# Optimization experiments

Measured on AMD Instinct MI355X. Metric: run time of the kernel, lower is better.

Reference implementation:

```python
import jax, jax.numpy as jnp
import numpy as np

KERNEL_SIZE = 5  # k, local correlation window
EPS = 1e-6


def local_self_correlation(x, k):
    """x: (b,c,h,w) -> (b,k^2,h,w). For each of the k^2 shifts (dy,dx) compute
    sum_c x[..., y+dy, x+dx] * x[..., y, x] with zero padding at borders."""
    pad = k // 2
    b, c, h, w = x.shape
    xp = jnp.pad(x, ((0, 0), (0, 0), (pad, pad), (pad, pad)))
    outs = []
    for dy in range(-pad, pad + 1):  # fixed small loop over k^2 shifts
        for dx in range(-pad, pad + 1):
            nb = xp[:, :, pad + dy:pad + dy + h, pad + dx:pad + dx + w]
            outs.append(jnp.sum(nb * x, axis=1))  # (b,h,w)
    return jnp.stack(outs, axis=1)  # (b,k^2,h,w)


def feature_l2norm(f):
    norm = jnp.sqrt(jnp.sum(f * f, axis=1, keepdims=True) + EPS)
    return f / norm


def setup_inputs() -> dict:
    key = jax.random.key(0)
    k1, k2, k3 = jax.random.split(key, 3)
    b, c, h, w = 8, 1024, 64, 64
    hidden = 1024
    in_dim = c + KERNEL_SIZE * KERNEL_SIZE  # 1049
    x = jax.random.normal(k1, (b, c, h, w), dtype=jnp.float32)
    W = jax.random.normal(k2, (hidden, in_dim), dtype=jnp.float32) * 0.02
    bias = jax.random.normal(k3, (hidden,), dtype=jnp.float32) * 0.02
    return {"x": x, "W": W, "b": bias}


def reference(x, W, b):
    feature_gs = local_self_correlation(x, KERNEL_SIZE)      # (b,k^2,h,w)
    feature_gs = feature_l2norm(feature_gs)
    feature_cat = jnp.concatenate([x, feature_gs], axis=1)    # (b,c+k^2,h,w)
    # 1x1 conv == channel GEMM, then ReLU
    out = jnp.einsum('bihw,oi->bohw', feature_cat, W) + b[None, :, None, None]
    return jax.nn.relu(out)
```

## Files before the change

kernel.cpp:

```cpp
#include <hip/hip_runtime.h>

typedef __attribute__((ext_vector_type(8))) short bf16x8;
typedef __attribute__((ext_vector_type(4))) float f32x4;

__device__ __forceinline__ unsigned short f2bf(float f) {
    unsigned int u = __float_as_uint(f);
    unsigned int r = (u + 0x7fffu + ((u >> 16) & 1u)) >> 16;
    return (unsigned short)r;
}

#define KPAD 1088
#define NT   17

__global__ void kWb_conv(const float* __restrict__ W, unsigned short* __restrict__ Wb)
{
    const int o = blockIdx.x;
    for (int k = threadIdx.x; k < KPAD; k += 256) {
        float v = (k < 1049) ? W[(size_t)o * 1049 + k] : 0.f;
        Wb[(size_t)o * KPAD + k] = f2bf(v);
    }
}

__global__ __launch_bounds__(256) void kT_conv(const float* __restrict__ x,
                                               unsigned short* __restrict__ xT)
{
    __shared__ unsigned short tile[64][128];
    const int bid = blockIdx.x;
    const int mst = bid >> 3;
    const int ct  = bid & 7;
    const int m0  = mst * 64;
    const int b   = m0 >> 12, ms0 = m0 & 4095;
    const int t   = threadIdx.x;
    const int msq = (t & 15) * 4;
    const int cg  = t >> 4;
    const int c0  = ct * 128 + cg * 8;

    const float* src = x + ((size_t)b * 1024 + c0) * 4096 + ms0 + msq;
    float4 v[8];
    #pragma unroll
    for (int j = 0; j < 8; ++j)
        v[j] = *(const float4*)(src + (size_t)j * 4096);

    #pragma unroll
    for (int p = 0; p < 4; ++p) {
        unsigned int w[4];
        #pragma unroll
        for (int q = 0; q < 4; ++q) {
            float lo = ((const float*)&v[2 * q])[p];
            float hi = ((const float*)&v[2 * q + 1])[p];
            w[q] = (unsigned int)f2bf(lo) | ((unsigned int)f2bf(hi) << 16);
        }
        const int row = msq + p;
        const int pch = cg ^ ((row >> 2) & 15);
        *(uint4*)&tile[row][pch * 8] = make_uint4(w[0], w[1], w[2], w[3]);
    }
    __syncthreads();

    #pragma unroll
    for (int q = 0; q < 4; ++q) {
        const int flat = q * 256 + t;
        const int row  = flat >> 4, ch = flat & 15;
        const int pch  = ch ^ ((row >> 2) & 15);
        uint4 val = *(const uint4*)&tile[row][pch * 8];
        *(uint4*)((char*)xT + (size_t)(m0 + row) * (KPAD * 2) + (size_t)(ct * 128 + ch * 8) * 2) = val;
    }
}

__global__ __launch_bounds__(256, 2) void k1a_corr(const float* __restrict__ x,
                                                   float* __restrict__ fpart)
{
    __shared__ float slab[2][20][68];
    const int bid   = blockIdx.x;
    const int split = bid & 15;
    const int b     = (bid >> 4) & 7;
    const int rg    = bid >> 7;
    const int y0    = rg * 16;
    const int t     = threadIdx.x;
    const int tc    = t & 15, tr = t >> 4;
    const int cs    = tc * 4;

    if (t < 160) {
        int buf = t / 80, rem = t % 80;
        int r = rem >> 2, cc = rem & 3;
        slab[buf][r][(cc < 2) ? cc : (64 + cc)] = 0.f;
    }

    float acc[25][4];
    #pragma unroll
    for (int s = 0; s < 25; ++s)
        #pragma unroll
        for (int p = 0; p < 4; ++p) acc[s][p] = 0.f;

    const float* xb = x + ((size_t)b * 1024 + split * 64) * 4096;

    const int r0 = t >> 4,         c40 = t & 15;
    const int y0r0 = y0 - 2 + r0;
    const int r1 = (t + 256) >> 4, c41 = t & 15;
    const int y0r1 = y0 - 2 + r1;
    const bool has1 = (t < 64);

    #define K1A_LOAD(ch, VA, VB)                                                \
        {                                                                        \
            const float* s_ = xb + (size_t)(ch) * 4096;                          \
            VA = (y0r0 >= 0 && y0r0 < 64) ? *(const float4*)(s_ + y0r0 * 64 + c40 * 4) \
                                          : make_float4(0.f, 0.f, 0.f, 0.f);     \
            if (has1)                                                            \
                VB = (y0r1 >= 0 && y0r1 < 64) ? *(const float4*)(s_ + y0r1 * 64 + c41 * 4) \
                                              : make_float4(0.f, 0.f, 0.f, 0.f); \
        }
    #define K1A_WRITE(buf, VA, VB)                                               \
        {                                                                        \
            float2* d0 = (float2*)&slab[buf][r0][2 + c40 * 4];                   \
            d0[0] = make_float2(VA.x, VA.y);                                     \
            d0[1] = make_float2(VA.z, VA.w);                                     \
            if (has1) {                                                          \
                float2* d1 = (float2*)&slab[buf][r1][2 + c41 * 4];               \
                d1[0] = make_float2(VB.x, VB.y);                                 \
                d1[1] = make_float2(VB.z, VB.w);                                 \
            }                                                                    \
        }
    #define K1A_COMPUTE(buf)                                                     \
        {                                                                        \
            const float* base = &slab[buf][tr][cs];                              \
            float ctr[4], wf[8];                                                 \
            {                                                                    \
                const float4* pr = (const float4*)(base + 2 * 68);               \
                float4 a = pr[0], b4 = pr[1];                                    \
                wf[0]=a.x; wf[1]=a.y; wf[2]=a.z; wf[3]=a.w;                      \
                wf[4]=b4.x; wf[5]=b4.y; wf[6]=b4.z; wf[7]=b4.w;                  \
                ctr[0]=wf[2]; ctr[1]=wf[3]; ctr[2]=wf[4]; ctr[3]=wf[5];          \
                _Pragma("unroll")                                                \
                for (int dx = -2; dx <= 2; ++dx)                                 \
                    _Pragma("unroll")                                            \
                    for (int p = 0; p < 4; ++p)                                  \
                        acc[10 + dx + 2][p] += wf[p + 2 + dx] * ctr[p];          \
            }                                                                    \
            _Pragma("unroll")                                                    \
            for (int r = 0; r < 5; ++r) {                                        \
                if (r == 2) continue;                                            \
                const float4* pr = (const float4*)(base + r * 68);               \
                float4 a = pr[0], b4 = pr[1];                                    \
                wf[0]=a.x; wf[1]=a.y; wf[2]=a.z; wf[3]=a.w;                      \
                wf[4]=b4.x; wf[5]=b4.y; wf[6]=b4.z; wf[7]=b4.w;                  \
                _Pragma("unroll")                                                \
                for (int dx = -2; dx <= 2; ++dx)                                 \
                    _Pragma("unroll")                                            \
                    for (int p = 0; p < 4; ++p)                                  \
                        acc[r * 5 + dx + 2][p] += wf[p + 2 + dx] * ctr[p];       \
            }                                                                    \
        }

    float4 Sa0, Sa1, Sb0, Sb1;
    K1A_LOAD(0, Sa0, Sa1)
    K1A_LOAD(1, Sb0, Sb1)
    K1A_WRITE(0, Sa0, Sa1)
    K1A_LOAD(2, Sa0, Sa1)
    __syncthreads();

    for (int i = 0; i < 64; i += 2) {
        K1A_WRITE(1, Sb0, Sb1)
        K1A_LOAD(min(i + 3, 63), Sb0, Sb1)
        K1A_COMPUTE(0)
        __syncthreads();
        K1A_WRITE(0, Sa0, Sa1)
        K1A_LOAD(min(i + 4, 63), Sa0, Sa1)
        K1A_COMPUTE(1)
        __syncthreads();
    }
    #undef K1A_LOAD
    #undef K1A_WRITE
    #undef K1A_COMPUTE

    const int mbase = b * 4096 + (y0 + tr) * 64 + cs;
    #pragma unroll
    for (int s = 0; s < 25; ++s) {
        *(float4*)(fpart + (size_t)(split * 25 + s) * 32768 + mbase) =
            make_float4(acc[s][0], acc[s][1], acc[s][2], acc[s][3]);
    }
}

__global__ void k1b_norm(const float* __restrict__ fpart, unsigned short* __restrict__ xT)
{
    const int m = blockIdx.x * 256 + threadIdx.x;
    float f[25];
    #pragma unroll
    for (int s = 0; s < 25; ++s) {
        float v = 0.f;
        #pragma unroll
        for (int sp = 0; sp < 16; ++sp)
            v += fpart[(size_t)(sp * 25 + s) * 32768 + m];
        f[s] = v;
    }
    float ss = 1e-6f;
    #pragma unroll
    for (int s = 0; s < 25; ++s) ss += f[s] * f[s];
    const float inv = 1.f / sqrtf(ss);

    unsigned int w[16];
    #pragma unroll
    for (int q = 0; q < 16; ++q) w[q] = 0u;
    #pragma unroll
    for (int s = 0; s < 25; ++s) {
        unsigned int h = f2bf(f[s] * inv);
        w[s >> 1] |= h << ((s & 1) * 16);
    }
    uint4* dst = (uint4*)((char*)xT + (size_t)m * (KPAD * 2) + 2048);
    dst[0] = make_uint4(w[0],  w[1],  w[2],  w[3]);
    dst[1] = make_uint4(w[4],  w[5],  w[6],  w[7]);
    dst[2] = make_uint4(w[8],  w[9],  w[10], w[11]);
    dst[3] = make_uint4(w[12], w[13], w[14], w[15]);
    uint4 z = make_uint4(0u, 0u, 0u, 0u);
    dst[4] = z; dst[5] = z; dst[6] = z; dst[7] = z;
}

__global__ __launch_bounds__(512, 2) void kgemm(const unsigned short* __restrict__ xT,
                                                const unsigned short* __restrict__ Wb,
                                                const float* __restrict__ bias,
                                                float* __restrict__ out)
{
    __shared__ unsigned short LA[2][256][64];
    __shared__ unsigned short LB[2][256][64];

    const int bid = blockIdx.x;
    const int wg  = (bid & 7) * 64 + (bid >> 3);
    const int mt  = wg >> 2, nt = wg & 3;
    const int m0  = mt * 256, n0 = nt * 256;
    const int t   = threadIdx.x;
    const int l   = t & 63, w = t >> 6;
    const int lr  = l & 15, kq = l >> 4;
    const int wm  = w >> 2, wn = w & 3;

    const int sr = l >> 3;
    const int sp = (l & 7) ^ sr;
    const unsigned short* gA = xT + (size_t)(m0 + w * 8 + sr) * KPAD + sp * 8;
    const unsigned short* gB = Wb + (size_t)(n0 + w * 8 + sr) * KPAD + sp * 8;

    auto STAGE = [&](int tt, int half) {
        if ((unsigned)tt >= NT) return;
        const int db = tt & 1;
        const size_t ko = (size_t)tt * 64;
        if (half < 2) {
            const unsigned short* g = gA + (size_t)(half * 128) * KPAD + ko;
            __builtin_amdgcn_global_load_lds((const void*)g,
                (void*)&LA[db][half * 128 + w * 8][0], 16, 0, 0);
            __builtin_amdgcn_global_load_lds((const void*)(g + (size_t)64 * KPAD),
                (void*)&LA[db][half * 128 + 64 + w * 8][0], 16, 0, 0);
        } else {
            const int hb = half - 2;
            const unsigned short* g = gB + (size_t)(hb * 128) * KPAD + ko;
            __builtin_amdgcn_global_load_lds((const void*)g,
                (void*)&LB[db][hb * 128 + w * 8][0], 16, 0, 0);
            __builtin_amdgcn_global_load_lds((const void*)(g + (size_t)64 * KPAD),
                (void*)&LB[db][hb * 128 + 64 + w * 8][0], 16, 0, 0);
        }
    };

    f32x4 zero = {0.f, 0.f, 0.f, 0.f};
    f32x4 acc[8][4];
    #pragma unroll
    for (int i = 0; i < 8; ++i)
        #pragma unroll
        for (int j = 0; j < 4; ++j) acc[i][j] = zero;

    bf16x8 a0[4][2], a1[4][2], b0[2][2], b1[2][2];

    #define LDA(dst, dbuf, ih)                                                   \
        _Pragma("unroll")                                                        \
        for (int i = 0; i < 4; ++i) {                                            \
            _Pragma("unroll")                                                    \
            for (int ks = 0; ks < 2; ++ks) {                                     \
                const int row = wm * 128 + ((ih) * 4 + i) * 16 + lr;             \
                const int slot = (ks * 4 + kq) ^ (row & 7);                      \
                dst[i][ks] = *(const bf16x8*)&LA[dbuf][row][slot * 8];           \
            }                                                                    \
        }
    #define LDB(dst, dbuf, jh)                                                   \
        _Pragma("unroll")                                                        \
        for (int j = 0; j < 2; ++j) {                                            \
            _Pragma("unroll")                                                    \
            for (int ks = 0; ks < 2; ++ks) {                                     \
                const int row = wn * 64 + ((jh) * 2 + j) * 16 + lr;              \
                const int slot = (ks * 4 + kq) ^ (row & 7);                      \
                dst[j][ks] = *(const bf16x8*)&LB[dbuf][row][slot * 8];           \
            }                                                                    \
        }
    #define MM(A, B, i0, j0)                                                     \
        _Pragma("unroll")                                                        \
        for (int ks = 0; ks < 2; ++ks) {                                         \
            _Pragma("unroll")                                                    \
            for (int i = 0; i < 4; ++i) {                                        \
                _Pragma("unroll")                                                \
                for (int j = 0; j < 2; ++j)                                      \
                    acc[(i0) + i][(j0) + j] = __builtin_amdgcn_mfma_f32_16x16x32_bf16( \
                        A[i][ks], B[j][ks], acc[(i0) + i][(j0) + j], 0, 0, 0);   \
            }                                                                    \
        }
    #define BAR()   asm volatile("s_barrier" ::: "memory");
    #define LGKM0() asm volatile("s_waitcnt lgkmcnt(0)" ::: "memory");           \
                    __builtin_amdgcn_sched_barrier(0);

    STAGE(0, 0); STAGE(0, 1); STAGE(0, 2); STAGE(0, 3);
    STAGE(1, 0); STAGE(1, 1); STAGE(1, 2); STAGE(1, 3);
    asm volatile("s_waitcnt vmcnt(8)" ::: "memory");
    BAR()

    for (int tt = 0; tt < NT; ++tt) {
        const int db = tt & 1;
        LDA(a0, db, 0)
        LDB(b0, db, 0)
        BAR()
        LGKM0()
        __builtin_amdgcn_s_setprio(1);
        MM(a0, b0, 0, 0)
        __builtin_amdgcn_s_setprio(0);
        BAR()
        LDA(a1, db, 1)
        LDB(b1, db, 1)
        BAR()
        LGKM0()
        __builtin_amdgcn_s_setprio(1);
        MM(a0, b1, 0, 2)
        __builtin_amdgcn_s_setprio(0);
        BAR()
        STAGE(tt + 2, 2);
        STAGE(tt + 2, 3);
        BAR()
        LGKM0()
        __builtin_amdgcn_s_setprio(1);
        MM(a1, b0, 4, 0)
        __builtin_amdgcn_s_setprio(0);
        BAR()
        STAGE(tt + 2, 0);
        STAGE(tt + 2, 1);
        BAR()
        LGKM0()
        __builtin_amdgcn_s_setprio(1);
        MM(a1, b1, 4, 2)
        __builtin_amdgcn_s_setprio(0);
        if (tt + 2 < NT) {
            asm volatile("s_waitcnt vmcnt(8)" ::: "memory");
        } else {
            asm volatile("s_waitcnt vmcnt(0)" ::: "memory");
        }
        BAR()
    }

    const int bb = m0 >> 12;
    const int ms = (m0 & 4095) + wm * 128 + kq * 4;
    #pragma unroll
    for (int j = 0; j < 4; ++j) {
        const int n = n0 + wn * 64 + j * 16 + lr;
        const float bv = bias[n];
        float* ob = out + (size_t)bb * 4194304 + (size_t)n * 4096 + ms;
        #pragma unroll
        for (int i = 0; i < 8; ++i) {
            f32x4 v = acc[i][j];
            float4 o = make_float4(fmaxf(v[0] + bv, 0.f), fmaxf(v[1] + bv, 0.f),
                                   fmaxf(v[2] + bv, 0.f), fmaxf(v[3] + bv, 0.f));
            *(float4*)(ob + i * 16) = o;
        }
    }
    #undef LDA
    #undef LDB
    #undef MM
    #undef BAR
    #undef LGKM0
}

extern "C" void kernel_launch(void* const* d_in, const int* in_sizes, int n_in,
                              void* d_out, int out_size, void* d_ws, size_t ws_size,
                              hipStream_t stream)
{
    const float* x    = (const float*)d_in[0];
    const float* W    = (const float*)d_in[1];
    const float* bias = (const float*)d_in[2];
    float* out        = (float*)d_out;

    char* ws = (char*)d_ws;
    unsigned short* xT = (unsigned short*)ws;
    unsigned short* Wb = (unsigned short*)(ws + 71303168);
    float* fpart       = (float*)d_out;

    kWb_conv<<<1024, 256, 0, stream>>>(W, Wb);
    kT_conv <<<4096, 256, 0, stream>>>(x, xT);
    k1a_corr<<<512,  256, 0, stream>>>(x, fpart);
    k1b_norm<<<128,  256, 0, stream>>>(fpart, xT);
    kgemm   <<<512,  512, 0, stream>>>(xT, Wb, bias, out);
}
```

Before: 211.7 us.

## Re-stage GEMM main loop with finer-grained prefetch and 2x unroll

Rewrites the bf16 MFMA GEMM main loop so global-to-LDS prefetches are split. Halves 1 and 3 of the next tile are issued while the current tile's LDS fragments load, and halves 0 and 2 of the tile after are issued between later MFMA groups. The loop is unrolled by two so the double-buffer index is a compile-time constant. Several barriers and full waits are replaced by partial lgkmcnt and vmcnt waits, to overlap LDS reads, global loads and MFMA work more tightly. This adds a risk of LDS buffer hazards if the new staging order overlaps buffers that are still being read.

```diff
diff --git a/kernel.cpp b/kernel.cpp
--- a/kernel.cpp
+++ b/kernel.cpp
@@ -264,24 +264,24 @@
 
     bf16x8 a0[4][2], a1[4][2], b0[2][2], b1[2][2];
 
-    #define LDA(dst, dbuf, ih)                                                   \
+    #define LDA(dst, DB, ih)                                                     \
         _Pragma("unroll")                                                        \
         for (int i = 0; i < 4; ++i) {                                            \
             _Pragma("unroll")                                                    \
             for (int ks = 0; ks < 2; ++ks) {                                     \
                 const int row = wm * 128 + ((ih) * 4 + i) * 16 + lr;             \
                 const int slot = (ks * 4 + kq) ^ (row & 7);                      \
-                dst[i][ks] = *(const bf16x8*)&LA[dbuf][row][slot * 8];           \
-            }                                                                    \
-        }
-    #define LDB(dst, dbuf, jh)                                                   \
+                dst[i][ks] = *(const bf16x8*)&LA[DB][row][slot * 8];             \
+            }                                                                    \
+        }
+    #define LDB(dst, DB, jh)                                                     \
         _Pragma("unroll")                                                        \
         for (int j = 0; j < 2; ++j) {                                            \
             _Pragma("unroll")                                                    \
             for (int ks = 0; ks < 2; ++ks) {                                     \
                 const int row = wn * 64 + ((jh) * 2 + j) * 16 + lr;              \
                 const int slot = (ks * 4 + kq) ^ (row & 7);                      \
-                dst[j][ks] = *(const bf16x8*)&LB[dbuf][row][slot * 8];           \
+                dst[j][ks] = *(const bf16x8*)&LB[DB][row][slot * 8];             \
             }                                                                    \
         }
     #define MM(A, B, i0, j0)                                                     \
@@ -295,55 +295,67 @@
                         A[i][ks], B[j][ks], acc[(i0) + i][(j0) + j], 0, 0, 0);   \
             }                                                                    \
         }
-    #define BAR()   asm volatile("s_barrier" ::: "memory");
-    #define LGKM0() asm volatile("s_waitcnt lgkmcnt(0)" ::: "memory");           \
-                    __builtin_amdgcn_sched_barrier(0);
-
-    STAGE(0, 0); STAGE(0, 1); STAGE(0, 2); STAGE(0, 3);
-    STAGE(1, 0); STAGE(1, 1); STAGE(1, 2); STAGE(1, 3);
-    asm volatile("s_waitcnt vmcnt(8)" ::: "memory");
-    BAR()
-
-    for (int tt = 0; tt < NT; ++tt) {
-        const int db = tt & 1;
-        LDA(a0, db, 0)
-        LDB(b0, db, 0)
-        BAR()
-        LGKM0()
-        __builtin_amdgcn_s_setprio(1);
-        MM(a0, b0, 0, 0)
-        __builtin_amdgcn_s_setprio(0);
-        BAR()
-        LDA(a1, db, 1)
-        LDB(b1, db, 1)
-        BAR()
-        LGKM0()
-        __builtin_amdgcn_s_setprio(1);
-        MM(a0, b1, 0, 2)
-        __builtin_amdgcn_s_setprio(0);
-        BAR()
-        STAGE(tt + 2, 2);
-        STAGE(tt + 2, 3);
-        BAR()
-        LGKM0()
-        __builtin_amdgcn_s_setprio(1);
-        MM(a1, b0, 4, 0)
-        __builtin_amdgcn_s_setprio(0);
-        BAR()
-        STAGE(tt + 2, 0);
-        STAGE(tt + 2, 1);
-        BAR()
-        LGKM0()
-        __builtin_amdgcn_s_setprio(1);
-        MM(a1, b1, 4, 2)
-        __builtin_amdgcn_s_setprio(0);
-        if (tt + 2 < NT) {
-            asm volatile("s_waitcnt vmcnt(8)" ::: "memory");
-        } else {
-            asm volatile("s_waitcnt vmcnt(0)" ::: "memory");
-        }
-        BAR()
-    }
+
+    #define TILE(DB, TT)                                                         \
+    {                                                                            \
+        const int tti = (TT);                                                    \
+                      \
+        LDA(a0, DB, 0)                                                           \
+        LDB(b0, DB, 0)                                                           \
+        STAGE(tti + 1, 1);                                                       \
+        asm volatile("s_waitcnt lgkmcnt(8)" ::: "memory");                       \
+        __builtin_amdgcn_s_barrier();                                            \
+        asm volatile("s_waitcnt lgkmcnt(0)" ::: "memory");                       \
+        __builtin_amdgcn_sched_barrier(0);                                       \
+        __builtin_amdgcn_s_setprio(1);                                           \
+        MM(a0, b0, 0, 0)                                                         \
+        __builtin_amdgcn_s_setprio(0);                                           \
+        __builtin_amdgcn_s_barrier();                                            \
+                      \
+        LDA(a1, DB, 1)                                                           \
+        LDB(b1, DB, 1)                                                           \
+        STAGE(tti + 1, 3);                                                       \
+        asm volatile("s_waitcnt lgkmcnt(8)" ::: "memory");                       \
+        __builtin_amdgcn_s_barrier();                                            \
+        asm volatile("s_waitcnt lgkmcnt(0)" ::: "memory");                       \
+        __builtin_amdgcn_sched_barrier(0);                                       \
+        __builtin_amdgcn_s_setprio(1);                                           \
+        MM(a0, b1, 0, 2)                                                         \
+        __builtin_amdgcn_s_setprio(0);                                           \
+        __builtin_amdgcn_s_barrier();                                            \
+            \
+        STAGE(tti + 2, 0);                                                       \
+        __builtin_amdgcn_s_barrier();                                            \
+        __builtin_amdgcn_s_setprio(1);                                           \
+        MM(a1, b0, 4, 0)                                                         \
+        __builtin_amdgcn_s_setprio(0);                                           \
+        __builtin_amdgcn_s_barrier();                                            \
+             \
+        STAGE(tti + 2, 2);                                                       \
+        __builtin_amdgcn_s_barrier();                                            \
+        __builtin_amdgcn_s_setprio(1);                                           \
+        MM(a1, b1, 4, 2)                                                         \
+        __builtin_amdgcn_s_setprio(0);                                           \
+        if (tti + 2 < NT) {                                                      \
+            asm volatile("s_waitcnt vmcnt(4)" ::: "memory");                     \
+        } else {                                                                 \
+            asm volatile("s_waitcnt vmcnt(0)" ::: "memory");                     \
+        }                                                                        \
+        __builtin_amdgcn_s_barrier();                                            \
+    }
+
+    STAGE(0, 0); STAGE(0, 2); STAGE(0, 1); STAGE(0, 3);
+    STAGE(1, 0); STAGE(1, 2);
+    asm volatile("s_waitcnt vmcnt(4)" ::: "memory");
+    __builtin_amdgcn_s_barrier();
+
+    int tt = 0;
+    #pragma unroll 1
+    for (int it = 0; it < (NT - 1) / 2; ++it, tt += 2) {
+        TILE(0, tt)
+        TILE(1, tt + 1)
+    }
+    TILE(0, NT - 1)
 
     const int bb = m0 >> 12;
     const int ms = (m0 & 4095) + wm * 128 + kq * 4;
@@ -363,8 +375,7 @@
     #undef LDA
     #undef LDB
     #undef MM
-    #undef BAR
-    #undef LGKM0
+    #undef TILE
 }
 
 extern "C" void kernel_launch(void* const* d_in, const int* in_sizes, int n_in,
```

New measurement: 203.5 us. 3.9% less time.
